# Optimization experiments

Measured on AMD Instinct MI355X. Metric: run time of the kernel, lower is better.

The kernel has to match this reference:

```python
import jax, jax.numpy as jnp
import numpy as np

HIDDEN = 16  # hidden_channels; conv outputs 3*HIDDEN gate channels

def setup_inputs() -> dict:
    key = jax.random.key(0)
    k1, k2 = jax.random.split(key)
    inputs = jax.random.normal(k1, (4, 16, 31, 128, 128), dtype=jnp.float32)
    # Conv3d weight (O, I, D, H, W); scaled down so tanh/sigmoid gates are not saturated
    W = jax.random.normal(k2, (3 * HIDDEN, 16, 3, 3, 3), dtype=jnp.float32) * 0.05
    b = jnp.zeros((3 * HIDDEN,), dtype=jnp.float32)
    return {"inputs": inputs, "W": W, "b": b}

def reference(inputs, W, b):
    # conv step: Conv3d with padding=1 (SAME for kernel 3, stride 1)
    gates = jax.lax.conv_general_dilated(
        inputs, W, window_strides=(1, 1, 1), padding='SAME',
        dimension_numbers=('NCDHW', 'OIDHW', 'NCDHW'))
    gates = gates + b[None, :, None, None, None]
    Z, F, O = jnp.split(gates, 3, axis=1)
    Z = jnp.tanh(Z)
    F = jax.nn.sigmoid(F)
    O = jax.nn.sigmoid(O)
    # fo-pooling: sequential linear recurrence over time axis (dim 2)
    Zt = jnp.moveaxis(Z, 2, 0)  # (T, N, C, H, W)
    Ft = jnp.moveaxis(F, 2, 0)
    Ot = jnp.moveaxis(O, 2, 0)
    c0 = jnp.zeros_like(Zt[0])  # c=None at t=0 is equivalent to c0=0

    def step(c, zfo):
        z, f, o = zfo
        c = f * c + (1.0 - f) * z
        return c, o * c

    _, h = jax.lax.scan(step, c0, (Zt, Ft, Ot))
    return jnp.moveaxis(h, 0, 2)  # back to (N, C, T, H, W)
```

## Files before the change

### kernel.cpp

```cpp
#include <hip/hip_runtime.h>


typedef __attribute__((ext_vector_type(8))) short short8;
typedef __attribute__((ext_vector_type(4))) float float4v;

#define TD 31
#define HW (128 * 128)
#define LH 6
#define LW 34
#define UNITS (LH * 2 * LW)
#define NSLOT 4
#define SLOTB (UNITS * 16)
#define WUNITS (14 * 3 * 64)
#define SMEM_BYTES ((WUNITS + NSLOT * UNITS) * 16)

__device__ __forceinline__ short f2bf(float f) {
    unsigned u = __float_as_uint(f);
    u = (u + 0x7FFFu + ((u >> 16) & 1u)) >> 16;
    return (short)u;
}

__device__ __forceinline__ float frcp(float x) { return __builtin_amdgcn_rcpf(x); }

__device__ __forceinline__ unsigned cvtpk(float lo, float hi) {
    unsigned r;
    asm("v_cvt_pk_bf16_f32 %0, %1, %2" : "=v"(r) : "v"(lo), "v"(hi));
    return r;
}

#define BARRIER() asm volatile("s_waitcnt lgkmcnt(0)\n\ts_barrier" ::: "memory")

__global__ __launch_bounds__(256, 2) void qrnn_mfma4(
    const float* __restrict__ x,
    const float* __restrict__ wt,
    const float* __restrict__ bias,
    float* __restrict__ out)
{
    extern __shared__ short8 smem[];
    short8* wlds = smem;
    short8* ring = smem + WUNITS;

    const int tid  = threadIdx.x;
    const int lane = tid & 63;
    const int wv   = tid >> 6;
    const int q    = lane >> 4;
    const int px   = lane & 15;
    const int b    = blockIdx.x;
    const int n    = b >> 7;
    const int h0   = ((b >> 2) & 31) * 4;
    const int w0   = (b & 3) * 32;

    const float* xin = x + (size_t)n * (16 * TD * HW);

    for (int k = 0; k < 11; ++k) {
        int u = tid + k * 256;
        if (u < WUNITS) {
            int l = u & 63, rest = u >> 6;
            int g = rest % 3, s = rest / 3;
            int qq = l >> 4, m = l & 15;
            short8 a;
#pragma unroll
            for (int j = 0; j < 8; ++j) {
                int kk = s * 32 + qq * 8 + j;
                int tap = kk >> 4, ic = kk & 15;
                float v = (tap < 27) ? wt[((size_t)((g * 16 + m) * 16 + ic)) * 27 + tap] : 0.f;
                a[j] = f2bf(v);
            }
            wlds[u] = a;
        }
    }
    {
        short8 z = (short8)0;
        for (int k = 0; k < 7; ++k) {
            int u = tid + k * 256;
            if (u < NSLOT * UNITS) ring[u] = z;
        }
    }

    int  s_off[2][8];
    bool s_ok[2];
#pragma unroll
    for (int i = 0; i < 2; ++i) {
        int u    = tid + i * 256;
        int uu   = (u < UNITS) ? u : 0;
        int wp   = uu % LW;
        int rest = uu / LW;
        int ck   = rest & 1;
        int hp   = rest >> 1;
        int hh   = h0 + hp - 1;
        int ww   = w0 + wp - 1;
        s_ok[i] = (u < UNITS) && ((unsigned)hh < 128u) && ((unsigned)ww < 128u);
        int hc = hh < 0 ? 0 : (hh > 127 ? 127 : hh);
        int wc = ww < 0 ? 0 : (ww > 127 ? 127 : ww);
#pragma unroll
        for (int j = 0; j < 8; ++j)
            s_off[i][j] = ((ck * 8 + j) * TD) * HW + hc * 128 + wc;
    }

    float rvA[2][8], rvB[2][8];

    auto issue = [&](int tt, float (&rv)[2][8]) {
        const int tc = ((unsigned)tt >= 31u) ? 0 : tt;
        const float* basep = xin + (size_t)tc * HW;
#pragma unroll
        for (int i = 0; i < 2; ++i)
#pragma unroll
            for (int j = 0; j < 8; ++j)
                rv[i][j] = basep[s_off[i][j]];
    };

    auto lds_write = [&](int wu, float (&rv)[2][8], bool tz) {
        if (!tz) {
#pragma unroll
            for (int i = 0; i < 2; ++i) {
                if (s_ok[i]) {
                    union { short8 s; unsigned u[4]; } v;
#pragma unroll
                    for (int k = 0; k < 4; ++k)
                        v.u[k] = cvtpk(rv[i][2 * k], rv[i][2 * k + 1]);
                    ring[wu + tid + i * 256] = v.s;
                }
            }
        } else {
            short8 z = (short8)0;
#pragma unroll
            for (int i = 0; i < 2; ++i)
                if (s_ok[i]) ring[wu + tid + i * 256] = z;
        }
    };

    int roff[14];
#pragma unroll
    for (int s = 0; s < 14; ++s) {
        int T = 2 * s + (q >> 1); if (T > 26) T = 26;
        int kd = T / 9, rr = T - kd * 9, kh = rr / 3, kw = rr - kh * 3;
        roff[s] = (((wv + kh) * 2 + (q & 1)) * LW + px + kw) * 16;
    }
    const int kd4 = q >> 1;

    float4v bv[3];
#pragma unroll
    for (int g = 0; g < 3; ++g)
        bv[g] = (float4v){bias[g * 16 + q * 4 + 0], bias[g * 16 + q * 4 + 1],
                          bias[g * 16 + q * 4 + 2], bias[g * 16 + q * 4 + 3]};

    float* po = out + ((size_t)(n * 16 + q * 4) * TD) * HW
                    + (size_t)(h0 + wv) * 128 + w0 + px;
    float cst[2][4] = {{0.f,0.f,0.f,0.f},{0.f,0.f,0.f,0.f}};

    BARRIER();
    issue(0, rvA); lds_write(0 * UNITS, rvA, false);
    issue(1, rvA); lds_write(1 * UNITS, rvA, false);
    issue(2, rvA);
    BARRIER();

    auto body = [&](int t, int r0, int r1, int r2, int r3,
                    float (&rvW)[2][8], float (&rvI)[2][8]) {
        issue(t + 3, rvI);

        float4v acc[2][3];
#pragma unroll
        for (int g = 0; g < 3; ++g) { acc[0][g] = bv[g]; acc[1][g] = bv[g]; }

        const int pk[3] = {r0, r1, r2};
        constexpr int kdt[14] = {0,0,0,0, 0 , 1,1,1,1, 2,2,2,2,2};
        const char* ringb = (const char*)ring;
#pragma unroll
        for (int s = 0; s < 14; ++s) {
            int sb = (s == 4) ? (kd4 ? r1 : r0) : pk[kdt[s]];
            const short8* bp = (const short8*)(ringb + sb + roff[s]);
            short8 b0 = bp[0];
            short8 b1 = bp[16];
#pragma unroll
            for (int g = 0; g < 3; ++g) {
                short8 wf = wlds[(s * 3 + g) * 64 + lane];
                acc[0][g] = __builtin_amdgcn_mfma_f32_16x16x32_bf16(wf, b0, acc[0][g], 0, 0, 0);
                acc[1][g] = __builtin_amdgcn_mfma_f32_16x16x32_bf16(wf, b1, acc[1][g], 0, 0, 0);
            }
        }
        lds_write(r3 >> 4, rvW, t >= 29);

#pragma unroll
        for (int tile = 0; tile < 2; ++tile) {
#pragma unroll
            for (int r = 0; r < 4; ++r) {
                float az = acc[tile][0][r];
                float af = acc[tile][1][r];
                float ao = acc[tile][2][r];
                float z = 1.f - 2.f * frcp(__expf(2.f * az) + 1.f);
                float f = frcp(1.f + __expf(-af));
                float o = frcp(1.f + __expf(-ao));
                float c = f * cst[tile][r] + (1.f - f) * z;
                cst[tile][r] = c;
                po[(size_t)r * (TD * HW) + tile * 16] = o * c;
            }
        }
        po += HW;
        BARRIER();
    };

    int r0 = 3 * SLOTB, r1 = 0, r2 = SLOTB, r3 = 2 * SLOTB;
    for (int t = 0; t < 30; t += 2) {
        body(t,     r0, r1, r2, r3, rvA, rvB);
        body(t + 1, r1, r2, r3, r0, rvB, rvA);
        int a = r0, c = r1;
        r0 = r2; r1 = r3; r2 = a; r3 = c;
    }
    body(30, r0, r1, r2, r3, rvA, rvB);
}

extern "C" void kernel_launch(void* const* d_in, const int* in_sizes, int n_in,
                              void* d_out, int out_size, void* d_ws, size_t ws_size,
                              hipStream_t stream) {
    const float* x    = (const float*)d_in[0];
    const float* wt   = (const float*)d_in[1];
    const float* bias = (const float*)d_in[2];
    float* out = (float*)d_out;

    static bool configured = false;
    if (!configured) {
        hipFuncSetAttribute((const void*)qrnn_mfma4,
                            hipFuncAttributeMaxDynamicSharedMemorySize,
                            SMEM_BYTES);
        configured = true;
    }

    qrnn_mfma4<<<dim3(512), dim3(256), SMEM_BYTES, stream>>>(x, wt, bias, out);
}
```

Before: 290.1 us.

## Hold two gate weight sets in registers and single-buffer the prefetch

Moves the Z and F gate weight fragments into per-thread registers and keeps only the O-gate weights in LDS, which cuts LDS reads per MFMA step and shrinks shared memory. The time loop is also rolled into a single loop with one prefetch register set, writing the prefetched slice to LDS before issuing the next global load. Per-channel offsets shrink to one base offset per unit, saving registers. The trade-off is higher VGPR pressure from 28 short8 weight registers, which could cause spills or lower occupancy. The shorter gap between the global load and its consumption may also expose more load latency.

```diff
diff --git a/kernel.cpp b/kernel.cpp
--- a/kernel.cpp
+++ b/kernel.cpp
@@ -11,8 +11,7 @@
 #define UNITS (LH * 2 * LW)
 #define NSLOT 4
 #define SLOTB (UNITS * 16)
-#define WUNITS (14 * 3 * 64)
-#define SMEM_BYTES ((WUNITS + NSLOT * UNITS) * 16)
+#define W2UNITS (14 * 64)
 
 __device__ __forceinline__ short f2bf(float f) {
     unsigned u = __float_as_uint(f);
@@ -30,15 +29,14 @@
 
 #define BARRIER() asm volatile("s_waitcnt lgkmcnt(0)\n\ts_barrier" ::: "memory")
 
-__global__ __launch_bounds__(256, 2) void qrnn_mfma4(
+__global__ __launch_bounds__(256, 2) void qrnn_mfma5(
     const float* __restrict__ x,
     const float* __restrict__ wt,
     const float* __restrict__ bias,
     float* __restrict__ out)
 {
-    extern __shared__ short8 smem[];
-    short8* wlds = smem;
-    short8* ring = smem + WUNITS;
+    __shared__ short8 wlds2[W2UNITS];
+    __shared__ short8 ring[NSLOT * UNITS];
 
     const int tid  = threadIdx.x;
     const int lane = tid & 63;
@@ -52,21 +50,36 @@
 
     const float* xin = x + (size_t)n * (16 * TD * HW);
 
-    for (int k = 0; k < 11; ++k) {
+    short8 wreg[2][14];
+#pragma unroll
+    for (int g = 0; g < 2; ++g)
+#pragma unroll
+        for (int s = 0; s < 14; ++s) {
+            short8 a;
+#pragma unroll
+            for (int j = 0; j < 8; ++j) {
+                int kk = s * 32 + q * 8 + j;
+                int tap = kk >> 4, ic = kk & 15;
+                float v = (tap < 27) ? wt[((size_t)((g * 16 + px) * 16 + ic)) * 27 + tap] : 0.f;
+                a[j] = f2bf(v);
+            }
+            wreg[g][s] = a;
+        }
+
+    for (int k = 0; k < 4; ++k) {
         int u = tid + k * 256;
-        if (u < WUNITS) {
-            int l = u & 63, rest = u >> 6;
-            int g = rest % 3, s = rest / 3;
+        if (u < W2UNITS) {
+            int l = u & 63, s = u >> 6;
             int qq = l >> 4, m = l & 15;
             short8 a;
 #pragma unroll
             for (int j = 0; j < 8; ++j) {
                 int kk = s * 32 + qq * 8 + j;
                 int tap = kk >> 4, ic = kk & 15;
-                float v = (tap < 27) ? wt[((size_t)((g * 16 + m) * 16 + ic)) * 27 + tap] : 0.f;
+                float v = (tap < 27) ? wt[((size_t)((32 + m) * 16 + ic)) * 27 + tap] : 0.f;
                 a[j] = f2bf(v);
             }
-            wlds[u] = a;
+            wlds2[u] = a;
         }
     }
     {
@@ -77,7 +90,7 @@
         }
     }
 
-    int  s_off[2][8];
+    unsigned voff[2];
     bool s_ok[2];
 #pragma unroll
     for (int i = 0; i < 2; ++i) {
@@ -92,24 +105,23 @@
         s_ok[i] = (u < UNITS) && ((unsigned)hh < 128u) && ((unsigned)ww < 128u);
         int hc = hh < 0 ? 0 : (hh > 127 ? 127 : hh);
         int wc = ww < 0 ? 0 : (ww > 127 ? 127 : ww);
-#pragma unroll
-        for (int j = 0; j < 8; ++j)
-            s_off[i][j] = ((ck * 8 + j) * TD) * HW + hc * 128 + wc;
-    }
-
-    float rvA[2][8], rvB[2][8];
-
-    auto issue = [&](int tt, float (&rv)[2][8]) {
+        voff[i] = (unsigned)(ck * (8 * TD * HW) + hc * 128 + wc);
+    }
+
+    float rv[2][8];
+
+    auto issue = [&](int tt) {
         const int tc = ((unsigned)tt >= 31u) ? 0 : tt;
         const float* basep = xin + (size_t)tc * HW;
 #pragma unroll
-        for (int i = 0; i < 2; ++i)
-#pragma unroll
-            for (int j = 0; j < 8; ++j)
-                rv[i][j] = basep[s_off[i][j]];
+        for (int j = 0; j < 8; ++j) {
+            const float* bj = basep + (size_t)j * (TD * HW);
+            rv[0][j] = bj[voff[0]];
+            rv[1][j] = bj[voff[1]];
+        }
     };
 
-    auto lds_write = [&](int wu, float (&rv)[2][8], bool tz) {
+    auto lds_write = [&](int wu, bool tz) {
         if (!tz) {
 #pragma unroll
             for (int i = 0; i < 2; ++i) {
@@ -149,14 +161,15 @@
     float cst[2][4] = {{0.f,0.f,0.f,0.f},{0.f,0.f,0.f,0.f}};
 
     BARRIER();
-    issue(0, rvA); lds_write(0 * UNITS, rvA, false);
-    issue(1, rvA); lds_write(1 * UNITS, rvA, false);
-    issue(2, rvA);
+    issue(0); lds_write(0 * UNITS, false);
+    issue(1); lds_write(1 * UNITS, false);
+    issue(2);
     BARRIER();
 
-    auto body = [&](int t, int r0, int r1, int r2, int r3,
-                    float (&rvW)[2][8], float (&rvI)[2][8]) {
-        issue(t + 3, rvI);
+    int r0 = 3 * SLOTB, r1 = 0, r2 = SLOTB, r3 = 2 * SLOTB;
+    for (int t = 0; t < TD; ++t) {
+        lds_write(r3 >> 4, t >= 29);
+        issue(t + 3);
 
         float4v acc[2][3];
 #pragma unroll
@@ -169,16 +182,16 @@
         for (int s = 0; s < 14; ++s) {
             int sb = (s == 4) ? (kd4 ? r1 : r0) : pk[kdt[s]];
             const short8* bp = (const short8*)(ringb + sb + roff[s]);
+            short8 wf2 = wlds2[s * 64 + lane];
             short8 b0 = bp[0];
             short8 b1 = bp[16];
-#pragma unroll
-            for (int g = 0; g < 3; ++g) {
-                short8 wf = wlds[(s * 3 + g) * 64 + lane];
-                acc[0][g] = __builtin_amdgcn_mfma_f32_16x16x32_bf16(wf, b0, acc[0][g], 0, 0, 0);
-                acc[1][g] = __builtin_amdgcn_mfma_f32_16x16x32_bf16(wf, b1, acc[1][g], 0, 0, 0);
-            }
-        }
-        lds_write(r3 >> 4, rvW, t >= 29);
+            acc[0][0] = __builtin_amdgcn_mfma_f32_16x16x32_bf16(wreg[0][s], b0, acc[0][0], 0, 0, 0);
+            acc[1][0] = __builtin_amdgcn_mfma_f32_16x16x32_bf16(wreg[0][s], b1, acc[1][0], 0, 0, 0);
+            acc[0][1] = __builtin_amdgcn_mfma_f32_16x16x32_bf16(wreg[1][s], b0, acc[0][1], 0, 0, 0);
+            acc[1][1] = __builtin_amdgcn_mfma_f32_16x16x32_bf16(wreg[1][s], b1, acc[1][1], 0, 0, 0);
+            acc[0][2] = __builtin_amdgcn_mfma_f32_16x16x32_bf16(wf2, b0, acc[0][2], 0, 0, 0);
+            acc[1][2] = __builtin_amdgcn_mfma_f32_16x16x32_bf16(wf2, b1, acc[1][2], 0, 0, 0);
+        }
 
 #pragma unroll
         for (int tile = 0; tile < 2; ++tile) {
@@ -197,16 +210,8 @@
         }
         po += HW;
         BARRIER();
-    };
-
-    int r0 = 3 * SLOTB, r1 = 0, r2 = SLOTB, r3 = 2 * SLOTB;
-    for (int t = 0; t < 30; t += 2) {
-        body(t,     r0, r1, r2, r3, rvA, rvB);
-        body(t + 1, r1, r2, r3, r0, rvB, rvA);
-        int a = r0, c = r1;
-        r0 = r2; r1 = r3; r2 = a; r3 = c;
-    }
-    body(30, r0, r1, r2, r3, rvA, rvB);
+        int tmp = r0; r0 = r1; r1 = r2; r2 = r3; r3 = tmp;
+    }
 }
 
 extern "C" void kernel_launch(void* const* d_in, const int* in_sizes, int n_in,
@@ -217,13 +222,5 @@
     const float* bias = (const float*)d_in[2];
     float* out = (float*)d_out;
 
-    static bool configured = false;
-    if (!configured) {
-        hipFuncSetAttribute((const void*)qrnn_mfma4,
-                            hipFuncAttributeMaxDynamicSharedMemorySize,
-                            SMEM_BYTES);
-        configured = true;
-    }
-
-    qrnn_mfma4<<<dim3(512), dim3(256), SMEM_BYTES, stream>>>(x, wt, bias, out);
-}
+    qrnn_mfma5<<<dim3(512), dim3(256), 0, stream>>>(x, wt, bias, out);
+}
```

New measurement: 340.1 us. 17.2% more time.

## Compute two timesteps per iteration, sharing weight fragments and halving barriers

Applied to the files above, without the earlier changes.

The main loop now computes two consecutive timesteps' convolutions at once. Each weight fragment loaded from LDS feeds 12 MFMAs instead of 6, and there are two barriers per pair of steps instead of one per step. Two input slices are prefetched per iteration, the per-channel global offsets collapse to one base offset per unit, and the ring offsets are packed two per register to cut VGPR use. The cost is more live accumulators and registers, which may hurt occupancy or cause spills, plus coarser overlap between loads and compute.

```diff
diff --git a/kernel.cpp b/kernel.cpp
--- a/kernel.cpp
+++ b/kernel.cpp
@@ -30,7 +30,9 @@
 
 #define BARRIER() asm volatile("s_waitcnt lgkmcnt(0)\n\ts_barrier" ::: "memory")
 
-__global__ __launch_bounds__(256, 2) void qrnn_mfma4(
+#define MFMA(A, B, C) __builtin_amdgcn_mfma_f32_16x16x32_bf16((A), (B), (C), 0, 0, 0)
+
+__global__ __launch_bounds__(256, 2) void qrnn_mfma8(
     const float* __restrict__ x,
     const float* __restrict__ wt,
     const float* __restrict__ bias,
@@ -77,7 +79,7 @@
         }
     }
 
-    int  s_off[2][8];
+    unsigned voff[2];
     bool s_ok[2];
 #pragma unroll
     for (int i = 0; i < 2; ++i) {
@@ -92,21 +94,20 @@
         s_ok[i] = (u < UNITS) && ((unsigned)hh < 128u) && ((unsigned)ww < 128u);
         int hc = hh < 0 ? 0 : (hh > 127 ? 127 : hh);
         int wc = ww < 0 ? 0 : (ww > 127 ? 127 : ww);
-#pragma unroll
-        for (int j = 0; j < 8; ++j)
-            s_off[i][j] = ((ck * 8 + j) * TD) * HW + hc * 128 + wc;
-    }
-
-    float rvA[2][8], rvB[2][8];
+        voff[i] = (unsigned)(ck * (8 * TD * HW) + hc * 128 + wc);
+    }
+
+    float rvH[2][8], rvC[2][8];
 
     auto issue = [&](int tt, float (&rv)[2][8]) {
         const int tc = ((unsigned)tt >= 31u) ? 0 : tt;
         const float* basep = xin + (size_t)tc * HW;
 #pragma unroll
-        for (int i = 0; i < 2; ++i)
-#pragma unroll
-            for (int j = 0; j < 8; ++j)
-                rv[i][j] = basep[s_off[i][j]];
+        for (int j = 0; j < 8; ++j) {
+            const float* bj = basep + (size_t)j * (TD * HW);
+            rv[0][j] = bj[voff[0]];
+            rv[1][j] = bj[voff[1]];
+        }
     };
 
     auto lds_write = [&](int wu, float (&rv)[2][8], bool tz) {
@@ -129,12 +130,18 @@
         }
     };
 
-    int roff[14];
-#pragma unroll
-    for (int s = 0; s < 14; ++s) {
-        int T = 2 * s + (q >> 1); if (T > 26) T = 26;
-        int kd = T / 9, rr = T - kd * 9, kh = rr / 3, kw = rr - kh * 3;
-        roff[s] = (((wv + kh) * 2 + (q & 1)) * LW + px + kw) * 16;
+    int roffp[7];
+#pragma unroll
+    for (int s2 = 0; s2 < 7; ++s2) {
+        int r01[2];
+#pragma unroll
+        for (int e = 0; e < 2; ++e) {
+            int s = 2 * s2 + e;
+            int T = 2 * s + (q >> 1); if (T > 26) T = 26;
+            int kd = T / 9, rr = T - kd * 9, kh = rr / 3, kw = rr - kh * 3;
+            r01[e] = (((wv + kh) * 2 + (q & 1)) * LW + px + kw) * 16;
+        }
+        roffp[s2] = (r01[0] & 0xffff) | (r01[1] << 16);
     }
     const int kd4 = q >> 1;
 
@@ -148,38 +155,7 @@
                     + (size_t)(h0 + wv) * 128 + w0 + px;
     float cst[2][4] = {{0.f,0.f,0.f,0.f},{0.f,0.f,0.f,0.f}};
 
-    BARRIER();
-    issue(0, rvA); lds_write(0 * UNITS, rvA, false);
-    issue(1, rvA); lds_write(1 * UNITS, rvA, false);
-    issue(2, rvA);
-    BARRIER();
-
-    auto body = [&](int t, int r0, int r1, int r2, int r3,
-                    float (&rvW)[2][8], float (&rvI)[2][8]) {
-        issue(t + 3, rvI);
-
-        float4v acc[2][3];
-#pragma unroll
-        for (int g = 0; g < 3; ++g) { acc[0][g] = bv[g]; acc[1][g] = bv[g]; }
-
-        const int pk[3] = {r0, r1, r2};
-        constexpr int kdt[14] = {0,0,0,0, 0 , 1,1,1,1, 2,2,2,2,2};
-        const char* ringb = (const char*)ring;
-#pragma unroll
-        for (int s = 0; s < 14; ++s) {
-            int sb = (s == 4) ? (kd4 ? r1 : r0) : pk[kdt[s]];
-            const short8* bp = (const short8*)(ringb + sb + roff[s]);
-            short8 b0 = bp[0];
-            short8 b1 = bp[16];
-#pragma unroll
-            for (int g = 0; g < 3; ++g) {
-                short8 wf = wlds[(s * 3 + g) * 64 + lane];
-                acc[0][g] = __builtin_amdgcn_mfma_f32_16x16x32_bf16(wf, b0, acc[0][g], 0, 0, 0);
-                acc[1][g] = __builtin_amdgcn_mfma_f32_16x16x32_bf16(wf, b1, acc[1][g], 0, 0, 0);
-            }
-        }
-        lds_write(r3 >> 4, rvW, t >= 29);
-
+    auto activate = [&](float4v (&acc)[2][3]) {
 #pragma unroll
         for (int tile = 0; tile < 2; ++tile) {
 #pragma unroll
@@ -196,17 +172,81 @@
             }
         }
         po += HW;
-        BARRIER();
     };
+
+    BARRIER();
+    issue(0, rvH); lds_write(0 * UNITS, rvH, false);
+    issue(1, rvH); lds_write(1 * UNITS, rvH, false);
+    issue(2, rvH); lds_write(2 * UNITS, rvH, false);
+    issue(3, rvH);
+    issue(4, rvC);
+    BARRIER();
 
     int r0 = 3 * SLOTB, r1 = 0, r2 = SLOTB, r3 = 2 * SLOTB;
     for (int t = 0; t < 30; t += 2) {
-        body(t,     r0, r1, r2, r3, rvA, rvB);
-        body(t + 1, r1, r2, r3, r0, rvB, rvA);
-        int a = r0, c = r1;
-        r0 = r2; r1 = r3; r2 = a; r3 = c;
-    }
-    body(30, r0, r1, r2, r3, rvA, rvB);
+        float4v accA[2][3], accB[2][3];
+#pragma unroll
+        for (int g = 0; g < 3; ++g) {
+            accA[0][g] = bv[g]; accA[1][g] = bv[g];
+            accB[0][g] = bv[g]; accB[1][g] = bv[g];
+        }
+
+        const int rr[4] = {r0, r1, r2, r3};
+        constexpr int kdt[14] = {0,0,0,0, 0 , 1,1,1,1, 2,2,2,2,2};
+        const char* ringb = (const char*)ring;
+#pragma unroll
+        for (int s = 0; s < 14; ++s) {
+            int ro  = (roffp[s >> 1] >> ((s & 1) * 16)) & 0xffff;
+            int sbA = (s == 4) ? (kd4 ? r1 : r0) : rr[kdt[s]];
+            int sbB = (s == 4) ? (kd4 ? r2 : r1) : rr[kdt[s] + 1];
+            const short8* bpA = (const short8*)(ringb + sbA + ro);
+            const short8* bpB = (const short8*)(ringb + sbB + ro);
+            short8 wf0 = wlds[(s * 3 + 0) * 64 + lane];
+            short8 wf1 = wlds[(s * 3 + 1) * 64 + lane];
+            short8 wf2 = wlds[(s * 3 + 2) * 64 + lane];
+            short8 a0 = bpA[0], a1 = bpA[16];
+            accA[0][0] = MFMA(wf0, a0, accA[0][0]); accA[1][0] = MFMA(wf0, a1, accA[1][0]);
+            accA[0][1] = MFMA(wf1, a0, accA[0][1]); accA[1][1] = MFMA(wf1, a1, accA[1][1]);
+            accA[0][2] = MFMA(wf2, a0, accA[0][2]); accA[1][2] = MFMA(wf2, a1, accA[1][2]);
+            short8 c0 = bpB[0], c1 = bpB[16];
+            accB[0][0] = MFMA(wf0, c0, accB[0][0]); accB[1][0] = MFMA(wf0, c1, accB[1][0]);
+            accB[0][1] = MFMA(wf1, c0, accB[0][1]); accB[1][1] = MFMA(wf1, c1, accB[1][1]);
+            accB[0][2] = MFMA(wf2, c0, accB[0][2]); accB[1][2] = MFMA(wf2, c1, accB[1][2]);
+        }
+        BARRIER();
+        lds_write(r0 >> 4, rvH, (t + 3) >= 31);
+        lds_write(r1 >> 4, rvC, (t + 4) >= 31);
+        issue(t + 5, rvH);
+        issue(t + 6, rvC);
+        activate(accA);
+        activate(accB);
+        BARRIER();
+        int ta = r0, tb = r1;
+        r0 = r2; r1 = r3; r2 = ta; r3 = tb;
+    }
+
+    {
+        float4v acc[2][3];
+#pragma unroll
+        for (int g = 0; g < 3; ++g) { acc[0][g] = bv[g]; acc[1][g] = bv[g]; }
+        const int rr[4] = {r0, r1, r2, r3};
+        constexpr int kdt[14] = {0,0,0,0, 0, 1,1,1,1, 2,2,2,2,2};
+        const char* ringb = (const char*)ring;
+#pragma unroll
+        for (int s = 0; s < 14; ++s) {
+            int ro = (roffp[s >> 1] >> ((s & 1) * 16)) & 0xffff;
+            int sb = (s == 4) ? (kd4 ? r1 : r0) : rr[kdt[s]];
+            const short8* bp = (const short8*)(ringb + sb + ro);
+            short8 wf0 = wlds[(s * 3 + 0) * 64 + lane];
+            short8 wf1 = wlds[(s * 3 + 1) * 64 + lane];
+            short8 wf2 = wlds[(s * 3 + 2) * 64 + lane];
+            short8 b0 = bp[0], b1 = bp[16];
+            acc[0][0] = MFMA(wf0, b0, acc[0][0]); acc[1][0] = MFMA(wf0, b1, acc[1][0]);
+            acc[0][1] = MFMA(wf1, b0, acc[0][1]); acc[1][1] = MFMA(wf1, b1, acc[1][1]);
+            acc[0][2] = MFMA(wf2, b0, acc[0][2]); acc[1][2] = MFMA(wf2, b1, acc[1][2]);
+        }
+        activate(acc);
+    }
 }
 
 extern "C" void kernel_launch(void* const* d_in, const int* in_sizes, int n_in,
@@ -219,11 +259,11 @@
 
     static bool configured = false;
     if (!configured) {
-        hipFuncSetAttribute((const void*)qrnn_mfma4,
+        hipFuncSetAttribute((const void*)qrnn_mfma8,
                             hipFuncAttributeMaxDynamicSharedMemorySize,
                             SMEM_BYTES);
         configured = true;
     }
 
-    qrnn_mfma4<<<dim3(512), dim3(256), SMEM_BYTES, stream>>>(x, wt, bias, out);
-}
+    qrnn_mfma8<<<dim3(512), dim3(256), SMEM_BYTES, stream>>>(x, wt, bias, out);
+}
```

Result: slower. 300.5 us (+3.6%).

## Software-pipeline MFMA of next step with activation/recurrence of previous step

Applied to the files above, without the earlier changes.

Restructures the time loop so each iteration runs the MFMA convolution for step t while doing the transcendental gate activations and recurrence for step t-1, using double-buffered accumulators. The LDS write of the prefetched input now happens before the MFMAs, and a single register set holds global loads, addressed through one base offset per unit instead of eight precomputed offsets. Weight fragments are loaded up front per tap group. The goal is to hide the activation and store latency behind matrix work and to cut register pressure from offsets. The extra accumulator set raises register use, which could hurt occupancy at two blocks per CU.

```diff
diff --git a/kernel.cpp b/kernel.cpp
--- a/kernel.cpp
+++ b/kernel.cpp
@@ -30,7 +30,9 @@
 
 #define BARRIER() asm volatile("s_waitcnt lgkmcnt(0)\n\ts_barrier" ::: "memory")
 
-__global__ __launch_bounds__(256, 2) void qrnn_mfma4(
+#define MFMA(A, B, C) __builtin_amdgcn_mfma_f32_16x16x32_bf16((A), (B), (C), 0, 0, 0)
+
+__global__ __launch_bounds__(256, 2) void qrnn_mfma9(
     const float* __restrict__ x,
     const float* __restrict__ wt,
     const float* __restrict__ bias,
@@ -77,7 +79,7 @@
         }
     }
 
-    int  s_off[2][8];
+    unsigned voff[2];
     bool s_ok[2];
 #pragma unroll
     for (int i = 0; i < 2; ++i) {
@@ -92,24 +94,23 @@
         s_ok[i] = (u < UNITS) && ((unsigned)hh < 128u) && ((unsigned)ww < 128u);
         int hc = hh < 0 ? 0 : (hh > 127 ? 127 : hh);
         int wc = ww < 0 ? 0 : (ww > 127 ? 127 : ww);
-#pragma unroll
-        for (int j = 0; j < 8; ++j)
-            s_off[i][j] = ((ck * 8 + j) * TD) * HW + hc * 128 + wc;
-    }
-
-    float rvA[2][8], rvB[2][8];
-
-    auto issue = [&](int tt, float (&rv)[2][8]) {
+        voff[i] = (unsigned)(ck * (8 * TD * HW) + hc * 128 + wc);
+    }
+
+    float rv[2][8];
+
+    auto issue = [&](int tt) {
         const int tc = ((unsigned)tt >= 31u) ? 0 : tt;
         const float* basep = xin + (size_t)tc * HW;
 #pragma unroll
-        for (int i = 0; i < 2; ++i)
-#pragma unroll
-            for (int j = 0; j < 8; ++j)
-                rv[i][j] = basep[s_off[i][j]];
-    };
-
-    auto lds_write = [&](int wu, float (&rv)[2][8], bool tz) {
+        for (int j = 0; j < 8; ++j) {
+            const float* bj = basep + (size_t)j * (TD * HW);
+            rv[0][j] = bj[voff[0]];
+            rv[1][j] = bj[voff[1]];
+        }
+    };
+
+    auto lds_write = [&](int wu, bool tz) {
         if (!tz) {
 #pragma unroll
             for (int i = 0; i < 2; ++i) {
@@ -148,20 +149,13 @@
                     + (size_t)(h0 + wv) * 128 + w0 + px;
     float cst[2][4] = {{0.f,0.f,0.f,0.f},{0.f,0.f,0.f,0.f}};
 
-    BARRIER();
-    issue(0, rvA); lds_write(0 * UNITS, rvA, false);
-    issue(1, rvA); lds_write(1 * UNITS, rvA, false);
-    issue(2, rvA);
-    BARRIER();
-
-    auto body = [&](int t, int r0, int r1, int r2, int r3,
-                    float (&rvW)[2][8], float (&rvI)[2][8]) {
-        issue(t + 3, rvI);
-
-        float4v acc[2][3];
+    float4v accA[2][3], accB[2][3];
+
+    int r0 = 3 * SLOTB, r1 = 0, r2 = SLOTB, r3 = 2 * SLOTB;
+
+    auto do_mfma = [&](float4v (&acc)[2][3]) {
 #pragma unroll
         for (int g = 0; g < 3; ++g) { acc[0][g] = bv[g]; acc[1][g] = bv[g]; }
-
         const int pk[3] = {r0, r1, r2};
         constexpr int kdt[14] = {0,0,0,0, 0 , 1,1,1,1, 2,2,2,2,2};
         const char* ringb = (const char*)ring;
@@ -169,17 +163,18 @@
         for (int s = 0; s < 14; ++s) {
             int sb = (s == 4) ? (kd4 ? r1 : r0) : pk[kdt[s]];
             const short8* bp = (const short8*)(ringb + sb + roff[s]);
+            short8 wf0 = wlds[(s * 3 + 0) * 64 + lane];
+            short8 wf1 = wlds[(s * 3 + 1) * 64 + lane];
+            short8 wf2 = wlds[(s * 3 + 2) * 64 + lane];
             short8 b0 = bp[0];
             short8 b1 = bp[16];
-#pragma unroll
-            for (int g = 0; g < 3; ++g) {
-                short8 wf = wlds[(s * 3 + g) * 64 + lane];
-                acc[0][g] = __builtin_amdgcn_mfma_f32_16x16x32_bf16(wf, b0, acc[0][g], 0, 0, 0);
-                acc[1][g] = __builtin_amdgcn_mfma_f32_16x16x32_bf16(wf, b1, acc[1][g], 0, 0, 0);
-            }
-        }
-        lds_write(r3 >> 4, rvW, t >= 29);
-
+            acc[0][0] = MFMA(wf0, b0, acc[0][0]); acc[1][0] = MFMA(wf0, b1, acc[1][0]);
+            acc[0][1] = MFMA(wf1, b0, acc[0][1]); acc[1][1] = MFMA(wf1, b1, acc[1][1]);
+            acc[0][2] = MFMA(wf2, b0, acc[0][2]); acc[1][2] = MFMA(wf2, b1, acc[1][2]);
+        }
+    };
+
+    auto activate = [&](float4v (&acc)[2][3]) {
 #pragma unroll
         for (int tile = 0; tile < 2; ++tile) {
 #pragma unroll
@@ -196,17 +191,38 @@
             }
         }
         po += HW;
+    };
+
+    auto rotate = [&]() { int tmp = r0; r0 = r1; r1 = r2; r2 = r3; r3 = tmp; };
+
+    BARRIER();
+    issue(0); lds_write(0 * UNITS, false);
+    issue(1); lds_write(1 * UNITS, false);
+    issue(2);
+    BARRIER();
+
+    lds_write(r3 >> 4, false);
+    issue(3);
+    do_mfma(accA);
+    BARRIER();
+    rotate();
+
+    for (int t = 1; t < 30; t += 2) {
+        lds_write(r3 >> 4, t >= 29);
+        issue(t + 3);
+        do_mfma(accB);
+        activate(accA);
         BARRIER();
-    };
-
-    int r0 = 3 * SLOTB, r1 = 0, r2 = SLOTB, r3 = 2 * SLOTB;
-    for (int t = 0; t < 30; t += 2) {
-        body(t,     r0, r1, r2, r3, rvA, rvB);
-        body(t + 1, r1, r2, r3, r0, rvB, rvA);
-        int a = r0, c = r1;
-        r0 = r2; r1 = r3; r2 = a; r3 = c;
-    }
-    body(30, r0, r1, r2, r3, rvA, rvB);
+        rotate();
+        lds_write(r3 >> 4, (t + 1) >= 29);
+        issue(t + 4);
+        do_mfma(accA);
+        activate(accB);
+        BARRIER();
+        rotate();
+    }
+
+    activate(accA);
 }
 
 extern "C" void kernel_launch(void* const* d_in, const int* in_sizes, int n_in,
@@ -219,11 +235,11 @@
 
     static bool configured = false;
     if (!configured) {
-        hipFuncSetAttribute((const void*)qrnn_mfma4,
+        hipFuncSetAttribute((const void*)qrnn_mfma9,
                             hipFuncAttributeMaxDynamicSharedMemorySize,
                             SMEM_BYTES);
         configured = true;
     }
 
-    qrnn_mfma4<<<dim3(512), dim3(256), SMEM_BYTES, stream>>>(x, wt, bias, out);
-}
+    qrnn_mfma9<<<dim3(512), dim3(256), SMEM_BYTES, stream>>>(x, wt, bias, out);
+}
```

Result: no change. 289.4 us (-0.2%).
